# Kernel tuning notes

Hardware: AMD Instinct MI355X
Metric: run time of the kernel (lower is better)

The kernel has to match this reference:

```python
import jax, jax.numpy as jnp
import numpy as np

LN_EPS = 1e-5
D_HEAD = 64


def _layernorm(x, w, b):
    x = x - jnp.mean(x, axis=-1, keepdims=True)
    scale = jnp.sqrt(jnp.mean(x * x, axis=-1, keepdims=True) + LN_EPS)
    return (x / scale) * w + b


def setup_inputs() -> dict:
    key = jax.random.key(0)
    ks = jax.random.split(key, 6)
    B, S, D, H, Dh = 2, 2048, 1024, 16, D_HEAD
    std = 0.02
    return {
        "resid_pre": jax.random.normal(ks[0], (B, S, D), dtype=jnp.float32),
        "W_Q": jax.random.normal(ks[1], (H, D, Dh), dtype=jnp.float32) * std,
        "b_Q": jnp.zeros((H, Dh), dtype=jnp.float32),
        "W_K": jax.random.normal(ks[2], (H, D, Dh), dtype=jnp.float32) * std,
        "b_K": jnp.zeros((H, Dh), dtype=jnp.float32),
        "W_V": jax.random.normal(ks[3], (H, D, Dh), dtype=jnp.float32) * std,
        "b_V": jnp.zeros((H, Dh), dtype=jnp.float32),
        "W_O": jax.random.normal(ks[4], (H, Dh, D), dtype=jnp.float32) * std,
        "b_O": jnp.zeros((D,), dtype=jnp.float32),
        "ln1_w": jnp.ones((D,), dtype=jnp.float32),
        "ln1_b": jnp.zeros((D,), dtype=jnp.float32),
        "ln2_w": jnp.ones((D,), dtype=jnp.float32),
        "ln2_b": jnp.zeros((D,), dtype=jnp.float32),
    }


def reference(resid_pre, W_Q, b_Q, W_K, b_K, W_V, b_V, W_O, b_O,
              ln1_w, ln1_b, ln2_w, ln2_b):
    x = _layernorm(resid_pre, ln1_w, ln1_b)  # [B,S,D]
    # per-head projections: [B,S,H,Dh]
    q = jnp.einsum('hdk,bsd->bshk', W_Q, x) + b_Q
    k = jnp.einsum('hdk,bsd->bshk', W_K, x) + b_K
    v = jnp.einsum('hdk,bsd->bshk', W_V, x) + b_V
    scores = jnp.einsum('bqhk,bphk->bhqp', q, k) / jnp.sqrt(
        jnp.asarray(D_HEAD, dtype=q.dtype))  # [B,H,S,S]
    S = scores.shape[-1]
    # Faithful to source: masked positions are filled with 0.0 (IGNORE buffer),
    # NOT -inf, before softmax.
    causal = jnp.tril(jnp.ones((S, S), dtype=bool))
    scores = jnp.where(causal, scores, jnp.asarray(0.0, dtype=scores.dtype))
    pattern = jax.nn.softmax(scores, axis=-1)
    z = jnp.einsum('bhqp,bphk->bqhk', pattern, v)
    attn_out = jnp.einsum('bqhk,hkd->bqd', z, W_O) + b_O
    resid_mid = resid_pre + attn_out
    resid_post = resid_mid + _layernorm(resid_mid, ln2_w, ln2_b)
    return resid_post
```

## Files before the change

### kernel.cpp

```cpp
#include <hip/hip_runtime.h>


typedef __attribute__((ext_vector_type(8))) short bf16x8_t;
typedef __attribute__((ext_vector_type(4))) float f32x4_t;
typedef unsigned short u16;
typedef unsigned int u32;

#define GLOAD16(src, dst) \
  __builtin_amdgcn_global_load_lds((const __attribute__((address_space(1))) void*)(src), \
                                   (__attribute__((address_space(3))) void*)(dst), 16, 0, 0)

__device__ __forceinline__ u16 f2bf(float f) {
    u32 x = __float_as_uint(f);
    return (u16)((x + 0x7fffu + ((x >> 16) & 1u)) >> 16);
}
__device__ __forceinline__ float bf2f(u16 u) {
    return __uint_as_float(((u32)u) << 16);
}
__device__ __forceinline__ u16 f2bf_cvt(float f) {
    u32 r;
    asm("v_cvt_pk_bf16_f32 %0, %1, %1" : "=v"(r) : "v"(f));
    return (u16)r;
}

__global__ __launch_bounds__(256) void ln1_kernel(const float* __restrict__ in,
                                                  const float* __restrict__ w,
                                                  const float* __restrict__ b,
                                                  u16* __restrict__ out) {
    const int r = blockIdx.x, tid = threadIdx.x, lane = tid & 63, wv = tid >> 6;
    const float4* row = (const float4*)(in + (size_t)r * 1024);
    float4 v = row[tid];
    float s1 = v.x + v.y + v.z + v.w;
    float s2 = v.x * v.x + v.y * v.y + v.z * v.z + v.w * v.w;
#pragma unroll
    for (int d = 1; d < 64; d <<= 1) { s1 += __shfl_xor(s1, d, 64); s2 += __shfl_xor(s2, d, 64); }
    __shared__ float r1[4], r2[4];
    if (lane == 0) { r1[wv] = s1; r2[wv] = s2; }
    __syncthreads();
    s1 = r1[0] + r1[1] + r1[2] + r1[3];
    s2 = r2[0] + r2[1] + r2[2] + r2[3];
    const float mean = s1 * (1.f / 1024.f);
    const float var  = s2 * (1.f / 1024.f) - mean * mean;
    const float inv  = rsqrtf(var + 1e-5f);
    float4 wv4 = ((const float4*)w)[tid], bv4 = ((const float4*)b)[tid];
    ushort4 o;
    o.x = f2bf((v.x - mean) * inv * wv4.x + bv4.x);
    o.y = f2bf((v.y - mean) * inv * wv4.y + bv4.y);
    o.z = f2bf((v.z - mean) * inv * wv4.z + bv4.z);
    o.w = f2bf((v.w - mean) * inv * wv4.w + bv4.w);
    ((ushort4*)(out + (size_t)r * 1024))[tid] = o;
}

__global__ __launch_bounds__(256) void transpose_w(const float* __restrict__ In,
                                                   u16* __restrict__ Out,
                                                   int K_, int N_) {
    __shared__ float t[64][65];
    const int k0 = blockIdx.x * 64, n0 = blockIdx.y * 64, z = blockIdx.z, tid = threadIdx.x;
    In  += (size_t)z * K_ * N_;
    Out += (size_t)z * N_ * K_;
#pragma unroll
    for (int j = 0; j < 16; ++j) {
        int idx = tid + 256 * j; int rr = idx >> 6, cc = idx & 63;
        t[rr][cc] = In[(size_t)(k0 + rr) * N_ + n0 + cc];
    }
    __syncthreads();
#pragma unroll
    for (int j = 0; j < 16; ++j) {
        int idx = tid + 256 * j; int n = idx >> 6, k = idx & 63;
        Out[(size_t)(n0 + n) * K_ + k0 + k] = f2bf(t[k][n]);
    }
}

__device__ __forceinline__ void gemm_mainloop(const u16* __restrict__ A, const u16* __restrict__ Bm,
                                              int K, int rowA, int rowB,
                                              char* lA, char* lB, f32x4_t (&acc)[4][4]) {
    const int tid = threadIdx.x, lane = tid & 63, w = tid >> 6;
    const int wm = w >> 1, wn = w & 1, c = lane & 15, g = lane >> 4;
    const size_t strideB = (size_t)K * 2;
    const char* Ab = (const char*)A;
    const char* Bb = (const char*)Bm;
    const int nkt = K >> 6;
    for (int kt = 0; kt < nkt; ++kt) {
#pragma unroll
        for (int it = 0; it < 4; ++it) {
            int T = it * 256 + tid;
            int row = T >> 3;
            int off = ((T & 7) << 4) ^ ((row & 7) << 4);
            GLOAD16(Ab + (size_t)(rowA + row) * strideB + (kt << 7) + off, lA + T * 16);
            GLOAD16(Bb + (size_t)(rowB + row) * strideB + (kt << 7) + off, lB + T * 16);
        }
        __syncthreads();
#pragma unroll
        for (int kc = 0; kc < 2; ++kc) {
            bf16x8_t af[4], bfr[4];
#pragma unroll
            for (int ms = 0; ms < 4; ++ms) {
                int row = wm * 64 + ms * 16 + c;
                af[ms] = *(const bf16x8_t*)(lA + row * 128 + (((kc << 6) + (g << 4)) ^ ((row & 7) << 4)));
            }
#pragma unroll
            for (int ns = 0; ns < 4; ++ns) {
                int row = wn * 64 + ns * 16 + c;
                bfr[ns] = *(const bf16x8_t*)(lB + row * 128 + (((kc << 6) + (g << 4)) ^ ((row & 7) << 4)));
            }
            __builtin_amdgcn_s_setprio(1);
#pragma unroll
            for (int ms = 0; ms < 4; ++ms)
#pragma unroll
                for (int ns = 0; ns < 4; ++ns)
                    acc[ms][ns] = __builtin_amdgcn_mfma_f32_16x16x32_bf16(af[ms], bfr[ns], acc[ms][ns], 0, 0, 0);
            __builtin_amdgcn_s_setprio(0);
        }
        __syncthreads();
    }
}

__global__ __launch_bounds__(256) void gemm_qkv(const u16* __restrict__ A, const u16* __restrict__ Bm,
                                                const float* __restrict__ bQ, const float* __restrict__ bK,
                                                const float* __restrict__ bV,
                                                u16* __restrict__ Qo, u16* __restrict__ Ko,
                                                u16* __restrict__ Vo) {
    __shared__ char lA[16384], lB[16384];
    f32x4_t acc[4][4];
#pragma unroll
    for (int ms = 0; ms < 4; ++ms)
#pragma unroll
        for (int ns = 0; ns < 4; ++ns) acc[ms][ns] = (f32x4_t){0.f, 0.f, 0.f, 0.f};
    const int bm = blockIdx.x, bn = blockIdx.y;
    gemm_mainloop(A, Bm, 1024, bm * 128, bn * 128, lA, lB, acc);
    const int tid = threadIdx.x, lane = tid & 63, w = tid >> 6;
    const int wm = w >> 1, wn = w & 1, c = lane & 15, g = lane >> 4;
#pragma unroll
    for (int ms = 0; ms < 4; ++ms) {
#pragma unroll
        for (int ns = 0; ns < 4; ++ns) {
            int gcol = bn * 128 + wn * 64 + ns * 16 + c;
            int p = gcol >> 10;
            int rem = gcol & 1023;
            const float* bias = (p == 0) ? bQ : (p == 1) ? bK : bV;
            u16* dst = (p == 0) ? Qo : (p == 1) ? Ko : Vo;
            float bv = bias[rem];
            int h = rem >> 6, dh = rem & 63;
#pragma unroll
            for (int i = 0; i < 4; ++i) {
                int grow = bm * 128 + wm * 64 + ms * 16 + g * 4 + i;
                float val = acc[ms][ns][i] + bv;
                if (p == 0) val *= 0.18033688011112042f;
                int bb = grow >> 11, pos = grow & 2047;
                dst[((size_t)((bb << 4) + h) * 2048 + pos) * 64 + dh] = f2bf(val);
            }
        }
    }
}

__global__ __launch_bounds__(256) void vtrans_psum(const u16* __restrict__ V,
                                                   u16* __restrict__ Vt,
                                                   float* __restrict__ Psum) {
    const int tile = blockIdx.x, bh = blockIdx.y, tid = threadIdx.x;
    const int q = tid >> 6, cc = tid & 63;
    const u16* src = V + ((size_t)bh * 2048 + tile * 64) * 64;
    u16* dst = Vt + (size_t)bh * 64 * 2048;
    __shared__ u16 tt[64][65];
    __shared__ float ps[4][64];
    float part = 0.f;
#pragma unroll
    for (int j = 0; j < 16; ++j) {
        int rr = q + 4 * j;
        u16 val = src[(size_t)rr * 64 + cc];
        tt[rr][cc] = val;
        part += bf2f(val);
    }
    ps[q][cc] = part;
    __syncthreads();
#pragma unroll
    for (int j = 0; j < 16; ++j) {
        int idx = tid + 256 * j; int dh = idx >> 6, kk = idx & 63;
        dst[(size_t)dh * 2048 + tile * 64 + kk] = tt[kk][dh];
    }
    if (tid < 64)
        Psum[((size_t)bh * 32 + tile) * 64 + tid] = ps[0][tid] + ps[1][tid] + ps[2][tid] + ps[3][tid];
}

__global__ __launch_bounds__(64) void vsuffix(const float* __restrict__ Psum,
                                              float* __restrict__ Vsuf) {
    const int bh = blockIdx.x, dh = threadIdx.x;
    const float* ps = Psum + (size_t)bh * 32 * 64;
    float* suf = Vsuf + (size_t)bh * 33 * 64;
    float run = 0.f;
    suf[32 * 64 + dh] = 0.f;
    for (int t = 31; t >= 0; --t) {
        run += ps[t * 64 + dh];
        suf[t * 64 + dh] = run;
    }
}

__global__ __launch_bounds__(256) void attn_kernel(const u16* __restrict__ Q, const u16* __restrict__ Kb,
                                                   const u16* __restrict__ Vt, const float* __restrict__ Vsuf,
                                                   u16* __restrict__ Z) {
    __shared__ char lK[2][8192], lV[2][8192], lP[4][2048];
    const int tid = threadIdx.x, lane = tid & 63, w = tid >> 6, c = lane & 15, g = lane >> 4;
    const int logical = (blockIdx.x & 7) * 128 + (blockIdx.x >> 3);
    const int bh = logical >> 5;
    const int qt = 31 - (logical & 31);
    const char* Kp = (const char*)(Kb + (size_t)bh * 2048 * 64);
    const char* Vp = (const char*)(Vt + (size_t)bh * 64 * 2048);
    const u16* Qp = Q + (size_t)bh * 2048 * 64;

    const int qrow = qt * 64 + w * 16 + c;
    bf16x8_t qf0 = *(const bf16x8_t*)(Qp + (size_t)qrow * 64 + g * 8);
    bf16x8_t qf1 = *(const bf16x8_t*)(Qp + (size_t)qrow * 64 + 32 + g * 8);

    float m_[4], l_[4];
    f32x4_t zacc[4];
#pragma unroll
    for (int i = 0; i < 4; ++i) { m_[i] = 0.f; l_[i] = 0.f; }
#pragma unroll
    for (int jd = 0; jd < 4; ++jd) zacc[jd] = (f32x4_t){0.f, 0.f, 0.f, 0.f};

    const int nkv = qt + 1;
    auto STAGE = [&](int kv, int buf) {
#pragma unroll
        for (int it = 0; it < 2; ++it) {
            int T = it * 256 + tid;
            int row = T >> 3;
            int off = ((T & 7) << 4) ^ ((row & 7) << 4);
            GLOAD16(Kp + (size_t)(kv * 64 + row) * 128 + off, &lK[buf][0] + T * 16);
            GLOAD16(Vp + (size_t)row * 4096 + kv * 128 + off, &lV[buf][0] + T * 16);
        }
    };

    STAGE(0, 0);
    __syncthreads();

    for (int kv = 0; kv < nkv; ++kv) {
        const int cur = kv & 1;
        if (kv + 1 < nkv) STAGE(kv + 1, cur ^ 1);
        const char* K0 = &lK[cur][0];
        const char* V0 = &lV[cur][0];

        f32x4_t s[4];
        __builtin_amdgcn_s_setprio(1);
#pragma unroll
        for (int j = 0; j < 4; ++j) {
            int kr = j * 16 + c;
            bf16x8_t k0 = *(const bf16x8_t*)(K0 + kr * 128 + (((g << 4)) ^ ((kr & 7) << 4)));
            bf16x8_t k1 = *(const bf16x8_t*)(K0 + kr * 128 + ((64 + (g << 4)) ^ ((kr & 7) << 4)));
            f32x4_t zz = (f32x4_t){0.f, 0.f, 0.f, 0.f};
            s[j] = __builtin_amdgcn_mfma_f32_16x16x32_bf16(qf0, k0, zz, 0, 0, 0);
            s[j] = __builtin_amdgcn_mfma_f32_16x16x32_bf16(qf1, k1, s[j], 0, 0, 0);
        }
        __builtin_amdgcn_s_setprio(0);
        if (kv == qt) {
#pragma unroll
            for (int j = 0; j < 4; ++j)
#pragma unroll
                for (int i = 0; i < 4; ++i) {
                    int key = kv * 64 + j * 16 + c;
                    int qr = qt * 64 + w * 16 + g * 4 + i;
                    if (key > qr) s[j][i] = 0.f;
                }
        }
        float pm[4];
#pragma unroll
        for (int i = 0; i < 4; ++i)
            pm[i] = fmaxf(fmaxf(s[0][i], s[1][i]), fmaxf(s[2][i], s[3][i]));
        int ok = 1;
#pragma unroll
        for (int i = 0; i < 4; ++i) ok &= (pm[i] <= m_[i] + 11.f);
        if (__builtin_expect(__all(ok), 1)) {
#pragma unroll
            for (int j = 0; j < 4; ++j)
#pragma unroll
                for (int i = 0; i < 4; ++i) {
                    float p = exp2f(s[j][i] - m_[i]);
                    s[j][i] = p;
                    l_[i] += p;
                }
        } else {
            float mn[4], sc[4];
#pragma unroll
            for (int d = 1; d < 16; d <<= 1)
#pragma unroll
                for (int i = 0; i < 4; ++i) pm[i] = fmaxf(pm[i], __shfl_xor(pm[i], d, 64));
#pragma unroll
            for (int i = 0; i < 4; ++i) {
                mn[i] = fmaxf(m_[i], pm[i]);
                sc[i] = exp2f(m_[i] - mn[i]);
            }
#pragma unroll
            for (int j = 0; j < 4; ++j)
#pragma unroll
                for (int i = 0; i < 4; ++i) {
                    float p = exp2f(s[j][i] - mn[i]);
                    s[j][i] = p;
                }
#pragma unroll
            for (int i = 0; i < 4; ++i) {
                l_[i] = l_[i] * sc[i] + (s[0][i] + s[1][i] + s[2][i] + s[3][i]);
                m_[i] = mn[i];
            }
#pragma unroll
            for (int jd = 0; jd < 4; ++jd)
#pragma unroll
                for (int i = 0; i < 4; ++i) zacc[jd][i] *= sc[i];
        }

        char* Pw = lP[w];
#pragma unroll
        for (int j = 0; j < 4; ++j)
#pragma unroll
            for (int i = 0; i < 4; ++i) {
                int rq = g * 4 + i;
                *(u16*)(Pw + rq * 128 + (((j << 5) + (c << 1)) ^ ((rq & 7) << 4))) = f2bf_cvt(s[j][i]);
            }
        bf16x8_t pf[2];
#pragma unroll
        for (int kc = 0; kc < 2; ++kc)
            pf[kc] = *(const bf16x8_t*)(Pw + c * 128 + (((kc << 6) + (g << 4)) ^ ((c & 7) << 4)));
        __builtin_amdgcn_s_setprio(1);
#pragma unroll
        for (int jd = 0; jd < 4; ++jd) {
            int vr = jd * 16 + c;
#pragma unroll
            for (int kc = 0; kc < 2; ++kc) {
                bf16x8_t vf = *(const bf16x8_t*)(V0 + vr * 128 + (((kc << 6) + (g << 4)) ^ ((vr & 7) << 4)));
                zacc[jd] = __builtin_amdgcn_mfma_f32_16x16x32_bf16(pf[kc], vf, zacc[jd], 0, 0, 0);
            }
        }
        __builtin_amdgcn_s_setprio(0);
        __syncthreads();
    }

#pragma unroll
    for (int d = 1; d < 16; d <<= 1)
#pragma unroll
        for (int i = 0; i < 4; ++i) l_[i] += __shfl_xor(l_[i], d, 64);

    const int Cout = 2048 - nkv * 64;
    const float* suf = Vsuf + (size_t)bh * 33 * 64 + nkv * 64;
    float s0f[4], lf[4];
#pragma unroll
    for (int i = 0; i < 4; ++i) {
        s0f[i] = exp2f(-m_[i]);
        lf[i] = l_[i] + (float)Cout * s0f[i];
    }
    const int bb = bh >> 4, hh = bh & 15;
#pragma unroll
    for (int jd = 0; jd < 4; ++jd) {
        float sv = suf[jd * 16 + c];
#pragma unroll
        for (int i = 0; i < 4; ++i) {
            float z = (zacc[jd][i] + s0f[i] * sv) / lf[i];
            size_t rowz = (size_t)bb * 2048 + qt * 64 + w * 16 + g * 4 + i;
            Z[rowz * 1024 + hh * 64 + jd * 16 + c] = f2bf_cvt(z);
        }
    }
}

__global__ __launch_bounds__(256) void gemm_out64(const u16* __restrict__ A, const u16* __restrict__ Bm,
                                                  const float* __restrict__ bO,
                                                  const float* __restrict__ resid,
                                                  float* __restrict__ outMid) {
    __shared__ char lA[8192], lB[16384];
    f32x4_t acc[2][4];
#pragma unroll
    for (int ms = 0; ms < 2; ++ms)
#pragma unroll
        for (int ns = 0; ns < 4; ++ns) acc[ms][ns] = (f32x4_t){0.f, 0.f, 0.f, 0.f};
    const int bm = blockIdx.x, bn = blockIdx.y;
    const int tid = threadIdx.x, lane = tid & 63, w = tid >> 6;
    const int wm = w >> 1, wn = w & 1, c = lane & 15, g = lane >> 4;
    const char* Ab = (const char*)A;
    const char* Bb = (const char*)Bm;
    const int rowA0 = bm * 64, rowB0 = bn * 128;
    for (int kt = 0; kt < 16; ++kt) {
#pragma unroll
        for (int it = 0; it < 2; ++it) {
            int T = it * 256 + tid;
            int row = T >> 3;
            int off = ((T & 7) << 4) ^ ((row & 7) << 4);
            GLOAD16(Ab + (size_t)(rowA0 + row) * 2048 + (kt << 7) + off, lA + T * 16);
        }
#pragma unroll
        for (int it = 0; it < 4; ++it) {
            int T = it * 256 + tid;
            int row = T >> 3;
            int off = ((T & 7) << 4) ^ ((row & 7) << 4);
            GLOAD16(Bb + (size_t)(rowB0 + row) * 2048 + (kt << 7) + off, lB + T * 16);
        }
        __syncthreads();
#pragma unroll
        for (int kc = 0; kc < 2; ++kc) {
            bf16x8_t af[2], bfr[4];
#pragma unroll
            for (int ms = 0; ms < 2; ++ms) {
                int row = wm * 32 + ms * 16 + c;
                af[ms] = *(const bf16x8_t*)(lA + row * 128 + (((kc << 6) + (g << 4)) ^ ((row & 7) << 4)));
            }
#pragma unroll
            for (int ns = 0; ns < 4; ++ns) {
                int row = wn * 64 + ns * 16 + c;
                bfr[ns] = *(const bf16x8_t*)(lB + row * 128 + (((kc << 6) + (g << 4)) ^ ((row & 7) << 4)));
            }
            __builtin_amdgcn_s_setprio(1);
#pragma unroll
            for (int ms = 0; ms < 2; ++ms)
#pragma unroll
                for (int ns = 0; ns < 4; ++ns)
                    acc[ms][ns] = __builtin_amdgcn_mfma_f32_16x16x32_bf16(af[ms], bfr[ns], acc[ms][ns], 0, 0, 0);
            __builtin_amdgcn_s_setprio(0);
        }
        __syncthreads();
    }
#pragma unroll
    for (int ms = 0; ms < 2; ++ms) {
#pragma unroll
        for (int ns = 0; ns < 4; ++ns) {
            int gcol = bn * 128 + wn * 64 + ns * 16 + c;
            float bo = bO[gcol];
#pragma unroll
            for (int i = 0; i < 4; ++i) {
                int grow = bm * 64 + wm * 32 + ms * 16 + g * 4 + i;
                size_t o = (size_t)grow * 1024 + gcol;
                outMid[o] = acc[ms][ns][i] + bo + resid[o];
            }
        }
    }
}

__global__ __launch_bounds__(256) void ln2_kernel(const float* __restrict__ mid,
                                                  const float* __restrict__ w,
                                                  const float* __restrict__ b,
                                                  float* __restrict__ out) {
    const int r = blockIdx.x, tid = threadIdx.x, lane = tid & 63, wv = tid >> 6;
    const float4* row = (const float4*)(mid + (size_t)r * 1024);
    float4 v = row[tid];
    float s1 = v.x + v.y + v.z + v.w;
    float s2 = v.x * v.x + v.y * v.y + v.z * v.z + v.w * v.w;
#pragma unroll
    for (int d = 1; d < 64; d <<= 1) { s1 += __shfl_xor(s1, d, 64); s2 += __shfl_xor(s2, d, 64); }
    __shared__ float r1[4], r2[4];
    if (lane == 0) { r1[wv] = s1; r2[wv] = s2; }
    __syncthreads();
    s1 = r1[0] + r1[1] + r1[2] + r1[3];
    s2 = r2[0] + r2[1] + r2[2] + r2[3];
    const float mean = s1 * (1.f / 1024.f);
    const float var  = s2 * (1.f / 1024.f) - mean * mean;
    const float inv  = rsqrtf(var + 1e-5f);
    float4 wv4 = ((const float4*)w)[tid], bv4 = ((const float4*)b)[tid];
    float4 o;
    o.x = v.x + (v.x - mean) * inv * wv4.x + bv4.x;
    o.y = v.y + (v.y - mean) * inv * wv4.y + bv4.y;
    o.z = v.z + (v.z - mean) * inv * wv4.z + bv4.z;
    o.w = v.w + (v.w - mean) * inv * wv4.w + bv4.w;
    ((float4*)(out + (size_t)r * 1024))[tid] = o;
}

extern "C" void kernel_launch(void* const* d_in, const int* in_sizes, int n_in,
                              void* d_out, int out_size, void* d_ws, size_t ws_size,
                              hipStream_t stream) {
    const float* resid_pre = (const float*)d_in[0];
    const float* W_Q  = (const float*)d_in[1];
    const float* b_Q  = (const float*)d_in[2];
    const float* W_K  = (const float*)d_in[3];
    const float* b_K  = (const float*)d_in[4];
    const float* W_V  = (const float*)d_in[5];
    const float* b_V  = (const float*)d_in[6];
    const float* W_O  = (const float*)d_in[7];
    const float* b_O  = (const float*)d_in[8];
    const float* ln1_w = (const float*)d_in[9];
    const float* ln1_b = (const float*)d_in[10];
    const float* ln2_w = (const float*)d_in[11];
    const float* ln2_b = (const float*)d_in[12];

    char* ws = (char*)d_ws;
    const size_t MB = 1u << 20;
    u16*  x_bf   = (u16*)(ws + 0);
    u16*  WqkvT  = (u16*)(ws + 8 * MB);
    u16*  Qb     = (u16*)(ws + 16 * MB);
    u16*  Kb     = (u16*)(ws + 24 * MB);
    u16*  Vb     = (u16*)(ws + 32 * MB);
    u16*  Vt     = (u16*)(ws + 40 * MB);
    float* Vsuf  = (float*)(ws + 48 * MB);
    float* Psum  = (float*)(ws + 48 * MB + 512 * 1024);
    u16*  Zb     = (u16*)(ws + 49 * MB);
    u16*  WoT    = (u16*)(ws + 57 * MB);
    float* resid_mid = (float*)(ws + 0);

    ln1_kernel<<<dim3(4096), dim3(256), 0, stream>>>(resid_pre, ln1_w, ln1_b, x_bf);

    transpose_w<<<dim3(16, 1, 16), dim3(256), 0, stream>>>(W_Q, WqkvT,                1024, 64);
    transpose_w<<<dim3(16, 1, 16), dim3(256), 0, stream>>>(W_K, WqkvT + 1024 * 1024,  1024, 64);
    transpose_w<<<dim3(16, 1, 16), dim3(256), 0, stream>>>(W_V, WqkvT + 2048 * 1024,  1024, 64);
    transpose_w<<<dim3(16, 16, 1), dim3(256), 0, stream>>>(W_O, WoT, 1024, 1024);

    gemm_qkv<<<dim3(32, 24), dim3(256), 0, stream>>>(x_bf, WqkvT, b_Q, b_K, b_V, Qb, Kb, Vb);

    vtrans_psum<<<dim3(32, 32), dim3(256), 0, stream>>>(Vb, Vt, Psum);
    vsuffix<<<dim3(32), dim3(64), 0, stream>>>(Psum, Vsuf);

    attn_kernel<<<dim3(1024), dim3(256), 0, stream>>>(Qb, Kb, Vt, Vsuf, Zb);

    gemm_out64<<<dim3(64, 8), dim3(256), 0, stream>>>(Zb, WoT, b_O, resid_pre, resid_mid);

    ln2_kernel<<<dim3(4096), dim3(256), 0, stream>>>(resid_mid, ln2_w, ln2_b, (float*)d_out);
}
```

Baseline: 232.0 us.

## Split long causal attention tiles across two blocks and merge with combine kernel

Query tiles 16-31 (the longest causal KV ranges) are now split into two halves of the KV loop, each run by its own block. Each half writes its partial Z in bf16 plus the row max and row sum. A new combine kernel rescales and merges the halves and folds in the masked-zero suffix term. This shortens the critical path and balances load across CUs, at the cost of an extra launch, extra global traffic for the partials, and bf16 rounding of the partial accumulators.

```diff
diff --git a/kernel.cpp b/kernel.cpp
--- a/kernel.cpp
+++ b/kernel.cpp
@@ -196,12 +196,21 @@
 
 __global__ __launch_bounds__(256) void attn_kernel(const u16* __restrict__ Q, const u16* __restrict__ Kb,
                                                    const u16* __restrict__ Vt, const float* __restrict__ Vsuf,
-                                                   u16* __restrict__ Z) {
+                                                   u16* __restrict__ Z, u16* __restrict__ Zp,
+                                                   float* __restrict__ Mp, float* __restrict__ Lp) {
     __shared__ char lK[2][8192], lV[2][8192], lP[4][2048];
     const int tid = threadIdx.x, lane = tid & 63, w = tid >> 6, c = lane & 15, g = lane >> 4;
-    const int logical = (blockIdx.x & 7) * 128 + (blockIdx.x >> 3);
-    const int bh = logical >> 5;
-    const int qt = 31 - (logical & 31);
+    const int logical = (blockIdx.x & 7) * 192 + (blockIdx.x >> 3);
+    const int bh = logical / 48;
+    const int s48 = logical % 48;
+    int qt, half;
+    if (s48 < 32) { qt = 31 - (s48 >> 1); half = s48 & 1; }
+    else          { qt = 47 - s48;        half = -1;      }
+    const int nkv = qt + 1;
+    const int h1 = (nkv + 1) >> 1;
+    const int kv0 = (half == 1) ? h1 : 0;
+    const int kv1 = (half == 0) ? h1 : nkv;
+
     const char* Kp = (const char*)(Kb + (size_t)bh * 2048 * 64);
     const char* Vp = (const char*)(Vt + (size_t)bh * 64 * 2048);
     const u16* Qp = Q + (size_t)bh * 2048 * 64;
@@ -217,7 +226,6 @@
 #pragma unroll
     for (int jd = 0; jd < 4; ++jd) zacc[jd] = (f32x4_t){0.f, 0.f, 0.f, 0.f};
 
-    const int nkv = qt + 1;
     auto STAGE = [&](int kv, int buf) {
 #pragma unroll
         for (int it = 0; it < 2; ++it) {
@@ -229,12 +237,12 @@
         }
     };
 
-    STAGE(0, 0);
+    STAGE(kv0, 0);
     __syncthreads();
 
-    for (int kv = 0; kv < nkv; ++kv) {
-        const int cur = kv & 1;
-        if (kv + 1 < nkv) STAGE(kv + 1, cur ^ 1);
+    for (int kv = kv0; kv < kv1; ++kv) {
+        const int cur = (kv - kv0) & 1;
+        if (kv + 1 < kv1) STAGE(kv + 1, cur ^ 1);
         const char* K0 = &lK[cur][0];
         const char* V0 = &lV[cur][0];
 
@@ -336,24 +344,72 @@
 #pragma unroll
         for (int i = 0; i < 4; ++i) l_[i] += __shfl_xor(l_[i], d, 64);
 
-    const int Cout = 2048 - nkv * 64;
-    const float* suf = Vsuf + (size_t)bh * 33 * 64 + nkv * 64;
-    float s0f[4], lf[4];
-#pragma unroll
-    for (int i = 0; i < 4; ++i) {
-        s0f[i] = exp2f(-m_[i]);
-        lf[i] = l_[i] + (float)Cout * s0f[i];
-    }
     const int bb = bh >> 4, hh = bh & 15;
-#pragma unroll
-    for (int jd = 0; jd < 4; ++jd) {
-        float sv = suf[jd * 16 + c];
+    if (half < 0) {
+        const int Cout = 2048 - nkv * 64;
+        const float* suf = Vsuf + (size_t)bh * 33 * 64 + nkv * 64;
+        float s0f[4], lf[4];
 #pragma unroll
         for (int i = 0; i < 4; ++i) {
-            float z = (zacc[jd][i] + s0f[i] * sv) / lf[i];
-            size_t rowz = (size_t)bb * 2048 + qt * 64 + w * 16 + g * 4 + i;
-            Z[rowz * 1024 + hh * 64 + jd * 16 + c] = f2bf_cvt(z);
-        }
+            s0f[i] = exp2f(-m_[i]);
+            lf[i] = l_[i] + (float)Cout * s0f[i];
+        }
+#pragma unroll
+        for (int jd = 0; jd < 4; ++jd) {
+            float sv = suf[jd * 16 + c];
+#pragma unroll
+            for (int i = 0; i < 4; ++i) {
+                float z = (zacc[jd][i] + s0f[i] * sv) / lf[i];
+                size_t rowz = (size_t)bb * 2048 + qt * 64 + w * 16 + g * 4 + i;
+                Z[rowz * 1024 + hh * 64 + jd * 16 + c] = f2bf_cvt(z);
+            }
+        }
+    } else {
+        const int base = (half * 32 + bh) * 2048;
+        if (c == 0) {
+#pragma unroll
+            for (int i = 0; i < 4; ++i) {
+                int row = qt * 64 + w * 16 + g * 4 + i;
+                Mp[base + row] = m_[i];
+                Lp[base + row] = l_[i];
+            }
+        }
+#pragma unroll
+        for (int jd = 0; jd < 4; ++jd)
+#pragma unroll
+            for (int i = 0; i < 4; ++i) {
+                int row = qt * 64 + w * 16 + g * 4 + i;
+                Zp[((size_t)(base + row)) * 64 + jd * 16 + c] = f2bf_cvt(zacc[jd][i]);
+            }
+    }
+}
+
+__global__ __launch_bounds__(256) void attn_combine(const u16* __restrict__ Zp,
+                                                    const float* __restrict__ Mp,
+                                                    const float* __restrict__ Lp,
+                                                    const float* __restrict__ Vsuf,
+                                                    u16* __restrict__ Z) {
+    const int bid = blockIdx.x;
+    const int bh = bid >> 4, seg = bid & 15, tid = threadIdx.x;
+    const int row = 1024 + seg * 64 + (tid >> 2);
+    const int q4 = (tid & 3) * 16;
+    const int qt = row >> 6, nkv = qt + 1, Cout = 2048 - nkv * 64;
+    const int baseA = bh * 2048 + row, baseB = (32 + bh) * 2048 + row;
+    const float mA = Mp[baseA], lA = Lp[baseA];
+    const float mB = Mp[baseB], lB = Lp[baseB];
+    const float M = fmaxf(mA, mB);
+    const float sA = exp2f(mA - M), sB = exp2f(mB - M), s0 = exp2f(-M);
+    const float lf = lA * sA + lB * sB + (float)Cout * s0;
+    const float inv = 1.f / lf;
+    const u16* zA = Zp + (size_t)baseA * 64 + q4;
+    const u16* zB = Zp + (size_t)baseB * 64 + q4;
+    const float* suf = Vsuf + ((size_t)bh * 33 + nkv) * 64 + q4;
+    const int bb = bh >> 4, hh = bh & 15;
+    u16* dst = Z + ((size_t)bb * 2048 + row) * 1024 + hh * 64 + q4;
+#pragma unroll
+    for (int d = 0; d < 16; ++d) {
+        float z = (sA * bf2f(zA[d]) + sB * bf2f(zB[d]) + s0 * suf[d]) * inv;
+        dst[d] = f2bf_cvt(z);
     }
 }
 
@@ -477,6 +533,8 @@
     const size_t MB = 1u << 20;
     u16*  x_bf   = (u16*)(ws + 0);
     u16*  WqkvT  = (u16*)(ws + 8 * MB);
+    u16*  Zp     = (u16*)(ws + 0);
+    float* resid_mid = (float*)(ws + 0);
     u16*  Qb     = (u16*)(ws + 16 * MB);
     u16*  Kb     = (u16*)(ws + 24 * MB);
     u16*  Vb     = (u16*)(ws + 32 * MB);
@@ -485,7 +543,8 @@
     float* Psum  = (float*)(ws + 48 * MB + 512 * 1024);
     u16*  Zb     = (u16*)(ws + 49 * MB);
     u16*  WoT    = (u16*)(ws + 57 * MB);
-    float* resid_mid = (float*)(ws + 0);
+    float* Mp    = (float*)(ws + 59 * MB);
+    float* Lp    = (float*)(ws + 59 * MB + 512 * 1024);
 
     ln1_kernel<<<dim3(4096), dim3(256), 0, stream>>>(resid_pre, ln1_w, ln1_b, x_bf);
 
@@ -499,7 +558,8 @@
     vtrans_psum<<<dim3(32, 32), dim3(256), 0, stream>>>(Vb, Vt, Psum);
     vsuffix<<<dim3(32), dim3(64), 0, stream>>>(Psum, Vsuf);
 
-    attn_kernel<<<dim3(1024), dim3(256), 0, stream>>>(Qb, Kb, Vt, Vsuf, Zb);
+    attn_kernel<<<dim3(1536), dim3(256), 0, stream>>>(Qb, Kb, Vt, Vsuf, Zb, Zp, Mp, Lp);
+    attn_combine<<<dim3(512), dim3(256), 0, stream>>>(Zp, Mp, Lp, Vsuf, Zb);
 
     gemm_out64<<<dim3(64, 8), dim3(256), 0, stream>>>(Zb, WoT, b_O, resid_pre, resid_mid);
 
```

Result: no change. 231.9 us (-0.0%).
